# Optimization experiments

Hardware: AMD Instinct MI355X
Metric: run time of the kernel (lower is better)

Reference implementation:

```python
import jax, jax.numpy as jnp
import numpy as np

B, N, M, D = 8, 2048, 2048, 512

def setup_inputs() -> dict:
    key = jax.random.key(0)
    ks = jax.random.split(key, 10)
    s = 1.0 / np.sqrt(D)  # torch Linear default init scale (approx)
    return {
        "lidar_features": jax.random.normal(ks[0], (B, N, D), jnp.float32),
        "camera_features": jax.random.normal(ks[1], (B, M, D), jnp.float32),
        "lidar_confidence": jax.random.uniform(ks[2], (B, N, 1), jnp.float32),
        "camera_confidence": jax.random.uniform(ks[3], (B, M, 1), jnp.float32),
        "Wq": jax.random.normal(ks[4], (D, D), jnp.float32) * s,
        "bq": jnp.zeros((D,), jnp.float32),
        "Wk": jax.random.normal(ks[5], (D, D), jnp.float32) * s,
        "bk": jnp.zeros((D,), jnp.float32),
        "Wv": jax.random.normal(ks[6], (D, D), jnp.float32) * s,
        "bv": jnp.zeros((D,), jnp.float32),
    }

def reference(lidar_features, camera_features, lidar_confidence, camera_confidence,
              Wq, bq, Wk, bk, Wv, bv):
    # torch nn.Linear: x @ W.T + b
    q = (jnp.einsum('bnd,ed->bne', lidar_features, Wq) + bq) * lidar_confidence
    k = jnp.einsum('bmd,ed->bme', camera_features, Wk) + bk
    v = jnp.einsum('bmd,ed->bme', camera_features, Wv) + bv
    # note: no 1/sqrt(d) scaling in the original; camera_confidence is unused
    scores = jnp.einsum('bne,bme->bnm', q, k)  # [B,N,M]
    attn = jax.nn.softmax(scores, axis=-1)
    fused = jnp.einsum('bnm,bme->bne', attn, v)
    return fused
```

## Files before the change

kernel.cpp:

```cpp
#include <hip/hip_runtime.h>
#include <hip/hip_bf16.h>

#define BB 8
#define NN 2048
#define MM 2048
#define DD 512

typedef __attribute__((ext_vector_type(8))) _Float16 f16x8;
typedef __attribute__((ext_vector_type(4))) float f32x4;
typedef __attribute__((ext_vector_type(8))) unsigned short u16x8;

__device__ __forceinline__ unsigned short f2h(float x){
  union { _Float16 h; unsigned short u; } cv;
  cv.h = (_Float16)x;
  return cv.u;
}
__device__ __forceinline__ float h2f(unsigned short u){
  union { unsigned short u; _Float16 h; } cv;
  cv.u = u;
  return (float)cv.h;
}
__device__ __forceinline__ f32x4 mfmah(f16x8 a, f16x8 b, f32x4 c){
  return __builtin_amdgcn_mfma_f32_16x16x32_f16(a, b, c, 0, 0, 0);
}

#define GLD16(gp, lp) __builtin_amdgcn_global_load_lds( \
    (const __attribute__((address_space(1))) void*)(gp), \
    (__attribute__((address_space(3))) void*)(lp), 16, 0, 0)

#define WAITVM(n) __builtin_amdgcn_s_waitcnt(0xF70 | (n))

__device__ __forceinline__ void swz_xyz(int& bn, int& bm, int& bz){
  int f = ((int)blockIdx.z * (int)gridDim.y + (int)blockIdx.y) * (int)gridDim.x
        + (int)blockIdx.x;
  bz = f & 7;
  int r = f >> 3;
  bn = r % (int)gridDim.x;
  bm = r / (int)gridDim.x;
}

__global__ __launch_bounds__(256) void cvt16_kernel(const float* __restrict__ in,
    unsigned short* __restrict__ out, int n4){
  int i = blockIdx.x*256 + threadIdx.x;
  const int stride = gridDim.x*256;
  for (; i < n4; i += stride){
    float4 v = ((const float4*)in)[i];
    ushort4 h; h.x=f2h(v.x); h.y=f2h(v.y); h.z=f2h(v.z); h.w=f2h(v.w);
    ((ushort4*)out)[i] = h;
  }
}

__global__ __launch_bounds__(256) void cam_prep(const float* __restrict__ cam,
    const float* __restrict__ c2,
    unsigned short* __restrict__ camH,
    float* __restrict__ svec){
  const int t = threadIdx.x;
  const int l = t & 63;
  const size_t row = (size_t)blockIdx.x*4 + (t >> 6);
  const float4* r4 = (const float4*)(cam + row*DD);
  const float4* c4 = (const float4*)c2;
  float4 v0 = r4[l*2],   v1 = r4[l*2+1];
  float4 a0 = c4[l*2],   a1 = c4[l*2+1];
  float p = v0.x*a0.x + v0.y*a0.y + v0.z*a0.z + v0.w*a0.w
          + v1.x*a1.x + v1.y*a1.y + v1.z*a1.z + v1.w*a1.w;
  for (int o = 32; o; o >>= 1) p += __shfl_xor(p, o);
  if (l == 0) svec[row] = p;
  ushort4 h0; h0.x=f2h(v0.x); h0.y=f2h(v0.y); h0.z=f2h(v0.z); h0.w=f2h(v0.w);
  ushort4 h1; h1.x=f2h(v1.x); h1.y=f2h(v1.y); h1.z=f2h(v1.z); h1.w=f2h(v1.w);
  ushort4* dst = (ushort4*)(camH + row*DD);
  dst[l*2]   = h0;
  dst[l*2+1] = h1;
}

__global__ __launch_bounds__(256) void at_kernel(const float* __restrict__ Wq,
                                                 const float* __restrict__ Wk,
                                                 unsigned short* __restrict__ atH){
  const int i0 = blockIdx.x * 32, j0 = blockIdx.y * 32;
  __shared__ float q_s[32][33];
  __shared__ float k_s[32][33];
  const int t = threadIdx.x;
  const int tx = t & 15, ty = t >> 4;
  float acc[2][2] = {{0.f,0.f},{0.f,0.f}};
  for (int e0 = 0; e0 < DD; e0 += 32){
    __syncthreads();
#pragma unroll
    for (int p = 0; p < 4; ++p){
      int idx = t + 256*p;
      int e = idx >> 5, c = idx & 31;
      q_s[e][c] = Wq[(size_t)(e0+e)*DD + i0 + c];
      k_s[e][c] = Wk[(size_t)(e0+e)*DD + j0 + c];
    }
    __syncthreads();
#pragma unroll 8
    for (int e = 0; e < 32; ++e){
      float q0 = q_s[e][2*tx], q1 = q_s[e][2*tx+1];
      float k0 = k_s[e][2*ty], k1 = k_s[e][2*ty+1];
      acc[0][0] += k0*q0; acc[0][1] += k0*q1;
      acc[1][0] += k1*q0; acc[1][1] += k1*q1;
    }
  }
#pragma unroll
  for (int a = 0; a < 2; ++a)
#pragma unroll
    for (int b = 0; b < 2; ++b)
      atH[(size_t)(j0 + 2*ty + a)*DD + i0 + 2*tx + b] = f2h(acc[a][b]);
}

__global__ __launch_bounds__(256) void c2_kernel(const float* __restrict__ bq,
                                                 const float* __restrict__ Wk,
                                                 float* __restrict__ c2){
  int d = blockIdx.x * 256 + threadIdx.x;
  float a = 0.f;
  for (int e = 0; e < DD; ++e) a += bq[e] * Wk[(size_t)e*DD + d];
  c2[d] = a;
}

template<int MODE>
__global__ __launch_bounds__(256) void gemm_h128(
    const unsigned short* __restrict__ Ag, long sA, int lda,
    const unsigned short* __restrict__ Bg, long sB, int ldb,
    unsigned short* __restrict__ O, long sO, int ldo,
    const float* __restrict__ bias)
{
  __shared__ __attribute__((aligned(16))) unsigned short Ah[128][40];
  __shared__ __attribute__((aligned(16))) unsigned short Bh[128][40];

  int bn, bm, bz; swz_xyz(bn, bm, bz);
  const int t = threadIdx.x;
  const int lane = t & 63, w = t >> 6;
  const int wrow = w >> 1, wcol = w & 1;
  const int lr = lane & 15, lk = (lane >> 4) << 3;

  f32x4 acc[4][4];
#pragma unroll
  for (int m = 0; m < 4; ++m)
#pragma unroll
    for (int n = 0; n < 4; ++n){ f32x4 z = {0.f,0.f,0.f,0.f}; acc[m][n] = z; }

  const unsigned short* Ap = Ag + (size_t)bz*(size_t)sA + ((size_t)bm*128)*(size_t)lda;
  const unsigned short* Bp = Bg + (size_t)bz*(size_t)sB + ((size_t)bn*128)*(size_t)ldb;

  const int sr = t >> 2;
  const int sc = (t & 3) * 8;

  for (int k0 = 0; k0 < DD; k0 += 32){
    __syncthreads();
#pragma unroll
    for (int p = 0; p < 2; ++p){
      int r = sr + 64*p;
      *(u16x8*)&Ah[r][sc] = *(const u16x8*)(Ap + (size_t)r*lda + k0 + sc);
      *(u16x8*)&Bh[r][sc] = *(const u16x8*)(Bp + (size_t)r*ldb + k0 + sc);
    }
    __syncthreads();

    f16x8 af[4], bf[4];
#pragma unroll
    for (int m = 0; m < 4; ++m) af[m] = *(const f16x8*)&Ah[wrow*64 + m*16 + lr][lk];
#pragma unroll
    for (int n = 0; n < 4; ++n) bf[n] = *(const f16x8*)&Bh[wcol*64 + n*16 + lr][lk];
#pragma unroll
    for (int m = 0; m < 4; ++m)
#pragma unroll
      for (int n = 0; n < 4; ++n)
        acc[m][n] = mfmah(af[m], bf[n], acc[m][n]);
  }

  const int orow = bm*128 + wrow*64;
  const int ocol = bn*128 + wcol*64;
#pragma unroll
  for (int m = 0; m < 4; ++m){
#pragma unroll
    for (int n = 0; n < 4; ++n){
      int col  = ocol + n*16 + lr;
      int row0 = orow + m*16 + ((lane >> 4) << 2);
#pragma unroll
      for (int r = 0; r < 4; ++r){
        int row = row0 + r;
        float v = acc[m][n][r];
        if constexpr (MODE == 1) v += bias[row];
        O[(size_t)bz*(size_t)sO + (size_t)row*ldo + col] = f2h(v);
      }
    }
  }
}

__global__ __launch_bounds__(512) void gemm_scores(
    const unsigned short* __restrict__ Th, const unsigned short* __restrict__ camH,
    unsigned short* __restrict__ O,
    const float* __restrict__ conf, const float* __restrict__ svec)
{
  __shared__ unsigned short Ah[3][128][32];
  __shared__ unsigned short Bh[3][256][32];

  int bn, bm, bz; swz_xyz(bn, bm, bz);
  const int t = threadIdx.x;
  const int lane = t & 63, w = t >> 6;
  const int wrow = w >> 2, wcol = w & 3;
  const int lr = lane & 15;
  const int c4 = lane >> 4;

  const unsigned short* Ap = Th   + (size_t)bz*((size_t)NN*DD) + ((size_t)bm*128)*DD;
  const unsigned short* Bp = camH + (size_t)bz*((size_t)MM*DD) + ((size_t)bn*256)*DD;

  const int sar  = w*16 + (lane >> 2);
  const int salc = (lane & 3) ^ (sar & 3);
  const unsigned short* gA = Ap + (size_t)sar*DD + salc*8;
  const int sbr  = w*32 + (lane >> 2);
  const int sblc = (lane & 3) ^ (sbr & 3);
  const unsigned short* gB = Bp + (size_t)sbr*DD + sblc*8;

#define SC_STAGE(bufi, kofs) do {                                  \
    GLD16(gA + (kofs),                 &Ah[bufi][w*16     ][0]);   \
    GLD16(gB + (kofs),                 &Bh[bufi][w*32     ][0]);   \
    GLD16(gB + (kofs) + (size_t)16*DD, &Bh[bufi][w*32 + 16][0]);   \
  } while(0)

#define SC_COMPUTE(bufi) do {                                      \
    f16x8 af[4], bf[4];                                            \
    _Pragma("unroll")                                              \
    for (int m = 0; m < 4; ++m){                                   \
      int row = wrow*64 + m*16 + lr;                               \
      int pc  = c4 ^ (row & 3);                                    \
      af[m] = *(const f16x8*)&Ah[bufi][row][pc*8];                 \
    }                                                              \
    _Pragma("unroll")                                              \
    for (int n = 0; n < 4; ++n){                                   \
      int row = wcol*64 + n*16 + lr;                               \
      int pc  = c4 ^ (row & 3);                                    \
      bf[n] = *(const f16x8*)&Bh[bufi][row][pc*8];                 \
    }                                                              \
    __builtin_amdgcn_s_setprio(1);                                 \
    _Pragma("unroll")                                              \
    for (int m = 0; m < 4; ++m)                                    \
      _Pragma("unroll")                                            \
      for (int n = 0; n < 4; ++n)                                  \
        acc[m][n] = mfmah(af[m], bf[n], acc[m][n]);                \
    __builtin_amdgcn_s_setprio(0);                                 \
  } while(0)

  f32x4 acc[4][4];
#pragma unroll
  for (int m = 0; m < 4; ++m)
#pragma unroll
    for (int n = 0; n < 4; ++n){ f32x4 z = {0.f,0.f,0.f,0.f}; acc[m][n] = z; }

  SC_STAGE(0, 0);
  SC_STAGE(1, 32);

  for (int tt = 0; tt < 15; ++tt){
    WAITVM(3);
    __builtin_amdgcn_s_barrier();
    __builtin_amdgcn_sched_barrier(0);
    if (tt < 14) SC_STAGE((tt+2)%3, (size_t)(tt+2)*32);
    SC_COMPUTE(tt%3);
  }
  WAITVM(0);
  __builtin_amdgcn_s_barrier();
  __builtin_amdgcn_sched_barrier(0);
  SC_COMPUTE(0);
#undef SC_STAGE
#undef SC_COMPUTE

  const int orow0 = bm*128 + wrow*64;
  const int ocol0 = bn*256 + wcol*64;
  const size_t obase = (size_t)bz*((size_t)NN*MM);
#pragma unroll
  for (int m = 0; m < 4; ++m){
#pragma unroll
    for (int n = 0; n < 4; ++n){
      int col  = ocol0 + n*16 + lr;
      float sv = svec[bz*MM + col];
      int row0 = orow0 + m*16 + ((lane >> 4) << 2);
#pragma unroll
      for (int r = 0; r < 4; ++r){
        int row = row0 + r;
        O[obase + (size_t)row*MM + col]
            = f2h(conf[bz*NN + row] * (acc[m][n][r] + sv));
      }
    }
  }
}

__global__ __launch_bounds__(256) void softmax_h(unsigned short* __restrict__ scores){
  const size_t row = blockIdx.x;
  unsigned short* pr = scores + row * (size_t)MM;
  const int t = threadIdx.x;

  u16x8 v = ((const u16x8*)pr)[t];
  float x[8];
#pragma unroll
  for (int j = 0; j < 8; ++j) x[j] = h2f(v[j]);

  float mx = x[0];
#pragma unroll
  for (int j = 1; j < 8; ++j) mx = fmaxf(mx, x[j]);
  for (int o = 32; o; o >>= 1) mx = fmaxf(mx, __shfl_xor(mx, o));
  __shared__ float red[4];
  if ((t & 63) == 0) red[t >> 6] = mx;
  __syncthreads();
  mx = fmaxf(fmaxf(red[0], red[1]), fmaxf(red[2], red[3]));

  float e[8], s = 0.f;
#pragma unroll
  for (int j = 0; j < 8; ++j){ e[j] = __expf(x[j] - mx); s += e[j]; }
  for (int o = 32; o; o >>= 1) s += __shfl_xor(s, o);
  __syncthreads();
  if ((t & 63) == 0) red[t >> 6] = s;
  __syncthreads();
  float inv = 1.f / (red[0] + red[1] + red[2] + red[3]);

  u16x8 pv;
#pragma unroll
  for (int j = 0; j < 8; ++j) pv[j] = f2h(e[j] * inv);
  ((u16x8*)pr)[t] = pv;
}

__global__ __launch_bounds__(512) void gemm_pv(
    const unsigned short* __restrict__ P,
    const unsigned short* __restrict__ V,
    float* __restrict__ O)
{
  __shared__ unsigned short Ah[2][64][64];
  __shared__ unsigned short Bh[2][256][64];

  int bn, bm, bz; swz_xyz(bn, bm, bz);
  const int t = threadIdx.x;
  const int lane = t & 63, w = t >> 6;
  const int lr = lane & 15, lc0 = lane >> 4;

  const unsigned short* Ap = P + (size_t)bz*((size_t)NN*MM) + ((size_t)bm*64)*MM;
  const unsigned short* Bp = V + (size_t)bz*((size_t)DD*MM) + ((size_t)bn*256)*MM;

  const int arow = 8*w + (lane >> 3);
  const int alc  = (lane & 7) ^ (arow & 7);
  const unsigned short* gA = Ap + (size_t)arow*MM + alc*8;
  const int brow = 32*w + (lane >> 3);
  const int blc  = (lane & 7) ^ (brow & 7);
  const unsigned short* gB = Bp + (size_t)brow*MM + blc*8;

#define PV_STAGE(bufi, kofs) do {                                   \
    GLD16(gA + (kofs),                 &Ah[bufi][8*w][0]);          \
    GLD16(gB + (kofs),                 &Bh[bufi][32*w     ][0]);    \
    GLD16(gB + (kofs) + (size_t)8*MM,  &Bh[bufi][32*w +  8][0]);    \
    GLD16(gB + (kofs) + (size_t)16*MM, &Bh[bufi][32*w + 16][0]);    \
    GLD16(gB + (kofs) + (size_t)24*MM, &Bh[bufi][32*w + 24][0]);    \
  } while(0)

  f32x4 acc[4][2];
#pragma unroll
  for (int m = 0; m < 4; ++m)
#pragma unroll
    for (int n = 0; n < 2; ++n){ f32x4 z = {0.f,0.f,0.f,0.f}; acc[m][n] = z; }

  PV_STAGE(0, 0);
  WAITVM(0);
  __builtin_amdgcn_s_barrier();
  __builtin_amdgcn_sched_barrier(0);

  for (int tt = 0; tt < 32; ++tt){
    const int buf = tt & 1;
    if (tt < 31) PV_STAGE(buf^1, (size_t)(tt+1)*64);
    f16x8 af[4][2], bf[2][2];
#pragma unroll
    for (int m = 0; m < 4; ++m){
      int row = m*16 + lr;
#pragma unroll
      for (int ks = 0; ks < 2; ++ks){
        int pc = (ks*4 + lc0) ^ (row & 7);
        af[m][ks] = *(const f16x8*)&Ah[buf][row][pc*8];
      }
    }
#pragma unroll
    for (int n = 0; n < 2; ++n){
      int row = w*32 + n*16 + lr;
#pragma unroll
      for (int ks = 0; ks < 2; ++ks){
        int pc = (ks*4 + lc0) ^ (row & 7);
        bf[n][ks] = *(const f16x8*)&Bh[buf][row][pc*8];
      }
    }
    __builtin_amdgcn_s_setprio(1);
#pragma unroll
    for (int m = 0; m < 4; ++m)
#pragma unroll
      for (int n = 0; n < 2; ++n){
        acc[m][n] = mfmah(af[m][0], bf[n][0], acc[m][n]);
        acc[m][n] = mfmah(af[m][1], bf[n][1], acc[m][n]);
      }
    __builtin_amdgcn_s_setprio(0);

    WAITVM(0);
    __builtin_amdgcn_s_barrier();
    __builtin_amdgcn_sched_barrier(0);
  }
#undef PV_STAGE

  const int orow0 = bm*64;
  const int ocol0 = bn*256 + w*32;
#pragma unroll
  for (int m = 0; m < 4; ++m){
#pragma unroll
    for (int n = 0; n < 2; ++n){
      int col  = ocol0 + n*16 + lr;
      int row0 = orow0 + m*16 + ((lane >> 4) << 2);
#pragma unroll
      for (int r = 0; r < 4; ++r){
        int row = row0 + r;
        O[(size_t)bz*((size_t)NN*DD) + (size_t)row*DD + col] = acc[m][n][r];
      }
    }
  }
}

extern "C" void kernel_launch(void* const* d_in, const int* in_sizes, int n_in,
                              void* d_out, int out_size, void* d_ws, size_t ws_size,
                              hipStream_t stream) {
  const float* lidar  = (const float*)d_in[0];
  const float* camera = (const float*)d_in[1];
  const float* lconf  = (const float*)d_in[2];
  const float* Wq = (const float*)d_in[4];
  const float* bq = (const float*)d_in[5];
  const float* Wk = (const float*)d_in[6];
  const float* Wv = (const float*)d_in[8];
  const float* bv = (const float*)d_in[9];
  float* out = (float*)d_out;

  char* ws = (char*)d_ws;
  unsigned short* scores = (unsigned short*)(ws + 0);
  unsigned short* liH    = (unsigned short*)(ws + 0);
  unsigned short* atH    = (unsigned short*)(ws + 16777216);
  unsigned short* wvH    = (unsigned short*)(ws + 17301504);
  float*          c2     = (float*)(ws + 17825792);
  unsigned short* Th     = (unsigned short*)(ws + 134217728);
  unsigned short* camH   = (unsigned short*)(ws + 150994944);
  unsigned short* Vt     = (unsigned short*)(ws + 167772160);
  float*          svec   = (float*)(ws + 184549376);

  c2_kernel<<<dim3(2), 256, 0, stream>>>(bq, Wk, c2);
  cam_prep<<<dim3(BB*MM/4), 256, 0, stream>>>(camera, c2, camH, svec);
  cvt16_kernel<<<dim3(2048), 256, 0, stream>>>(lidar,  liH,  BB*NN*DD/4);
  cvt16_kernel<<<dim3(256),  256, 0, stream>>>(Wv,     wvH,  DD*DD/4);
  at_kernel<<<dim3(16,16), 256, 0, stream>>>(Wq, Wk, atH);

  gemm_h128<0><<<dim3(DD/128, NN/128, BB), 256, 0, stream>>>(
      liH, (long)NN*DD, DD,  atH, 0, DD,
      Th, (long)NN*DD, DD, nullptr);

  gemm_h128<1><<<dim3(MM/128, DD/128, BB), 256, 0, stream>>>(
      wvH, 0, DD,  camH, (long)MM*DD, DD,
      Vt, (long)DD*MM, MM, bv);

  gemm_scores<<<dim3(MM/256, NN/128, BB), 512, 0, stream>>>(
      Th, camH, scores, lconf, svec);

  softmax_h<<<dim3(BB*NN), 256, 0, stream>>>(scores);

  gemm_pv<<<dim3(DD/256, NN/64, BB), 512, 0, stream>>>(
      scores, Vt, out);
}
```

Before: 196.4 us.

## Enlarge PV GEMM tile to 128x256 with 4-stage shared-memory pipeline

The P·V GEMM block tile grows from 64x256 to 128x256, and the warps are rearranged as a 2x4 grid where each warp owns a 64x64 output subtile. This raises operand reuse from LDS and halves the number of re-reads of V per output row. The single double buffer with K-step 64 becomes a 4-stage ring with K-step 32 and partial vmcnt waits, so global loads run several steps ahead of compute. In exchange it uses more accumulator registers, and launches half as many blocks, which may reduce occupancy.

```diff
diff --git a/kernel.cpp b/kernel.cpp
--- a/kernel.cpp
+++ b/kernel.cpp
@@ -320,93 +320,100 @@
     const unsigned short* __restrict__ V,
     float* __restrict__ O)
 {
-  __shared__ unsigned short Ah[2][64][64];
-  __shared__ unsigned short Bh[2][256][64];
+  __shared__ unsigned short Ah[4][128][32];
+  __shared__ unsigned short Bh[4][256][32];
 
   int bn, bm, bz; swz_xyz(bn, bm, bz);
   const int t = threadIdx.x;
   const int lane = t & 63, w = t >> 6;
-  const int lr = lane & 15, lc0 = lane >> 4;
-
-  const unsigned short* Ap = P + (size_t)bz*((size_t)NN*MM) + ((size_t)bm*64)*MM;
+  const int wrow = w >> 2, wcol = w & 3;
+  const int lr = lane & 15;
+  const int c4 = lane >> 4;
+
+  const unsigned short* Ap = P + (size_t)bz*((size_t)NN*MM) + ((size_t)bm*128)*MM;
   const unsigned short* Bp = V + (size_t)bz*((size_t)DD*MM) + ((size_t)bn*256)*MM;
 
-  const int arow = 8*w + (lane >> 3);
-  const int alc  = (lane & 7) ^ (arow & 7);
-  const unsigned short* gA = Ap + (size_t)arow*MM + alc*8;
-  const int brow = 32*w + (lane >> 3);
-  const int blc  = (lane & 7) ^ (brow & 7);
-  const unsigned short* gB = Bp + (size_t)brow*MM + blc*8;
-
-#define PV_STAGE(bufi, kofs) do {                                   \
-    GLD16(gA + (kofs),                 &Ah[bufi][8*w][0]);          \
-    GLD16(gB + (kofs),                 &Bh[bufi][32*w     ][0]);    \
-    GLD16(gB + (kofs) + (size_t)8*MM,  &Bh[bufi][32*w +  8][0]);    \
-    GLD16(gB + (kofs) + (size_t)16*MM, &Bh[bufi][32*w + 16][0]);    \
-    GLD16(gB + (kofs) + (size_t)24*MM, &Bh[bufi][32*w + 24][0]);    \
+  const int sar  = w*16 + (lane >> 2);
+  const int salc = (lane & 3) ^ (sar & 3);
+  const unsigned short* gA = Ap + (size_t)sar*MM + salc*8;
+  const int sbr  = w*32 + (lane >> 2);
+  const int sblc = (lane & 3) ^ (sbr & 3);
+  const unsigned short* gB = Bp + (size_t)sbr*MM + sblc*8;
+
+#define PV_STAGE(bufi, kofs) do {                                  \
+    GLD16(gA + (kofs),                 &Ah[bufi][w*16     ][0]);   \
+    GLD16(gB + (kofs),                 &Bh[bufi][w*32     ][0]);   \
+    GLD16(gB + (kofs) + (size_t)16*MM, &Bh[bufi][w*32 + 16][0]);   \
   } while(0)
 
-  f32x4 acc[4][2];
+#define PV_COMPUTE(bufi) do {                                      \
+    f16x8 af[4], bf[4];                                            \
+    _Pragma("unroll")                                              \
+    for (int m = 0; m < 4; ++m){                                   \
+      int row = wrow*64 + m*16 + lr;                               \
+      int pc  = c4 ^ (row & 3);                                    \
+      af[m] = *(const f16x8*)&Ah[bufi][row][pc*8];                 \
+    }                                                              \
+    _Pragma("unroll")                                              \
+    for (int n = 0; n < 4; ++n){                                   \
+      int row = wcol*64 + n*16 + lr;                               \
+      int pc  = c4 ^ (row & 3);                                    \
+      bf[n] = *(const f16x8*)&Bh[bufi][row][pc*8];                 \
+    }                                                              \
+    __builtin_amdgcn_s_setprio(1);                                 \
+    _Pragma("unroll")                                              \
+    for (int m = 0; m < 4; ++m)                                    \
+      _Pragma("unroll")                                            \
+      for (int n = 0; n < 4; ++n)                                  \
+        acc[m][n] = mfmah(af[m], bf[n], acc[m][n]);                \
+    __builtin_amdgcn_s_setprio(0);                                 \
+  } while(0)
+
+  f32x4 acc[4][4];
 #pragma unroll
   for (int m = 0; m < 4; ++m)
 #pragma unroll
-    for (int n = 0; n < 2; ++n){ f32x4 z = {0.f,0.f,0.f,0.f}; acc[m][n] = z; }
+    for (int n = 0; n < 4; ++n){ f32x4 z = {0.f,0.f,0.f,0.f}; acc[m][n] = z; }
 
   PV_STAGE(0, 0);
+  PV_STAGE(1, 32);
+  PV_STAGE(2, 64);
+
+  for (int tt = 0; tt < 61; ++tt){
+    WAITVM(6);
+    __builtin_amdgcn_s_barrier();
+    __builtin_amdgcn_sched_barrier(0);
+    PV_STAGE((tt+3)&3, (size_t)(tt+3)*32);
+    PV_COMPUTE(tt&3);
+  }
+  WAITVM(6);
+  __builtin_amdgcn_s_barrier();
+  __builtin_amdgcn_sched_barrier(0);
+  PV_COMPUTE(1);
+  WAITVM(3);
+  __builtin_amdgcn_s_barrier();
+  __builtin_amdgcn_sched_barrier(0);
+  PV_COMPUTE(2);
   WAITVM(0);
   __builtin_amdgcn_s_barrier();
   __builtin_amdgcn_sched_barrier(0);
-
-  for (int tt = 0; tt < 32; ++tt){
-    const int buf = tt & 1;
-    if (tt < 31) PV_STAGE(buf^1, (size_t)(tt+1)*64);
-    f16x8 af[4][2], bf[2][2];
-#pragma unroll
-    for (int m = 0; m < 4; ++m){
-      int row = m*16 + lr;
-#pragma unroll
-      for (int ks = 0; ks < 2; ++ks){
-        int pc = (ks*4 + lc0) ^ (row & 7);
-        af[m][ks] = *(const f16x8*)&Ah[buf][row][pc*8];
-      }
-    }
-#pragma unroll
-    for (int n = 0; n < 2; ++n){
-      int row = w*32 + n*16 + lr;
-#pragma unroll
-      for (int ks = 0; ks < 2; ++ks){
-        int pc = (ks*4 + lc0) ^ (row & 7);
-        bf[n][ks] = *(const f16x8*)&Bh[buf][row][pc*8];
-      }
-    }
-    __builtin_amdgcn_s_setprio(1);
-#pragma unroll
-    for (int m = 0; m < 4; ++m)
-#pragma unroll
-      for (int n = 0; n < 2; ++n){
-        acc[m][n] = mfmah(af[m][0], bf[n][0], acc[m][n]);
-        acc[m][n] = mfmah(af[m][1], bf[n][1], acc[m][n]);
-      }
-    __builtin_amdgcn_s_setprio(0);
-
-    WAITVM(0);
-    __builtin_amdgcn_s_barrier();
-    __builtin_amdgcn_sched_barrier(0);
-  }
+  PV_COMPUTE(3);
 #undef PV_STAGE
-
-  const int orow0 = bm*64;
-  const int ocol0 = bn*256 + w*32;
+#undef PV_COMPUTE
+
+  const int orow0 = bm*128 + wrow*64;
+  const int ocol0 = bn*256 + wcol*64;
+  const size_t obase = (size_t)bz*((size_t)NN*DD);
 #pragma unroll
   for (int m = 0; m < 4; ++m){
 #pragma unroll
-    for (int n = 0; n < 2; ++n){
+    for (int n = 0; n < 4; ++n){
       int col  = ocol0 + n*16 + lr;
       int row0 = orow0 + m*16 + ((lane >> 4) << 2);
 #pragma unroll
       for (int r = 0; r < 4; ++r){
         int row = row0 + r;
-        O[(size_t)bz*((size_t)NN*DD) + (size_t)row*DD + col] = acc[m][n][r];
+        O[obase + (size_t)row*DD + col] = acc[m][n][r];
       }
     }
   }
@@ -455,6 +462,6 @@
 
   softmax_h<<<dim3(BB*NN), 256, 0, stream>>>(scores);
 
-  gemm_pv<<<dim3(DD/256, NN/64, BB), 512, 0, stream>>>(
+  gemm_pv<<<dim3(DD/256, NN/128, BB), 512, 0, stream>>>(
       scores, Vt, out);
 }
```

Result: slower. 216.7 us (+10.3%).

## Rewrite projection GEMMs with async double-buffered swizzled LDS pipeline

Applied to the files above, without the earlier changes.

The two projection GEMMs move from a 128x128 tile with synchronous global-to-LDS copies to a 64x256 tile with 512 threads, using direct global-to-LDS loads into double-buffered XOR-swizzled shared memory, the same scheme the PV kernel already uses. The next k-tile is prefetched while MFMAs run on the current one, and wave priority is raised around the MFMA block. This targets load latency and LDS bank conflicts in the Q-side and V projections. It also changes the tile shape and grid size, which affects occupancy and how often operands are reused.

```diff
diff --git a/kernel.cpp b/kernel.cpp
--- a/kernel.cpp
+++ b/kernel.cpp
@@ -116,63 +116,95 @@
 }
 
 template<int MODE>
-__global__ __launch_bounds__(256) void gemm_h128(
+__global__ __launch_bounds__(512) void gemm_h256(
     const unsigned short* __restrict__ Ag, long sA, int lda,
     const unsigned short* __restrict__ Bg, long sB, int ldb,
     unsigned short* __restrict__ O, long sO, int ldo,
     const float* __restrict__ bias)
 {
-  __shared__ __attribute__((aligned(16))) unsigned short Ah[128][40];
-  __shared__ __attribute__((aligned(16))) unsigned short Bh[128][40];
+  __shared__ unsigned short Ah[2][64][64];
+  __shared__ unsigned short Bh[2][256][64];
 
   int bn, bm, bz; swz_xyz(bn, bm, bz);
   const int t = threadIdx.x;
   const int lane = t & 63, w = t >> 6;
-  const int wrow = w >> 1, wcol = w & 1;
-  const int lr = lane & 15, lk = (lane >> 4) << 3;
-
-  f32x4 acc[4][4];
+  const int lr = lane & 15, lc0 = lane >> 4;
+
+  const unsigned short* Ap = Ag + (size_t)bz*(size_t)sA + ((size_t)bm*64)*(size_t)lda;
+  const unsigned short* Bp = Bg + (size_t)bz*(size_t)sB + ((size_t)bn*256)*(size_t)ldb;
+
+  const int arow = 8*w + (lane >> 3);
+  const int alc  = (lane & 7) ^ (arow & 7);
+  const unsigned short* gA = Ap + (size_t)arow*lda + alc*8;
+  const int brow = 32*w + (lane >> 3);
+  const int blc  = (lane & 7) ^ (brow & 7);
+  const unsigned short* gB = Bp + (size_t)brow*ldb + blc*8;
+
+#define H_STAGE(bufi, kofs) do {                                     \
+    GLD16(gA + (kofs),                  &Ah[bufi][8*w][0]);          \
+    GLD16(gB + (kofs),                  &Bh[bufi][32*w     ][0]);    \
+    GLD16(gB + (kofs) + (size_t)8*ldb,  &Bh[bufi][32*w +  8][0]);    \
+    GLD16(gB + (kofs) + (size_t)16*ldb, &Bh[bufi][32*w + 16][0]);    \
+    GLD16(gB + (kofs) + (size_t)24*ldb, &Bh[bufi][32*w + 24][0]);    \
+  } while(0)
+
+  f32x4 acc[4][2];
 #pragma unroll
   for (int m = 0; m < 4; ++m)
 #pragma unroll
-    for (int n = 0; n < 4; ++n){ f32x4 z = {0.f,0.f,0.f,0.f}; acc[m][n] = z; }
-
-  const unsigned short* Ap = Ag + (size_t)bz*(size_t)sA + ((size_t)bm*128)*(size_t)lda;
-  const unsigned short* Bp = Bg + (size_t)bz*(size_t)sB + ((size_t)bn*128)*(size_t)ldb;
-
-  const int sr = t >> 2;
-  const int sc = (t & 3) * 8;
-
-  for (int k0 = 0; k0 < DD; k0 += 32){
-    __syncthreads();
-#pragma unroll
-    for (int p = 0; p < 2; ++p){
-      int r = sr + 64*p;
-      *(u16x8*)&Ah[r][sc] = *(const u16x8*)(Ap + (size_t)r*lda + k0 + sc);
-      *(u16x8*)&Bh[r][sc] = *(const u16x8*)(Bp + (size_t)r*ldb + k0 + sc);
-    }
-    __syncthreads();
-
-    f16x8 af[4], bf[4];
-#pragma unroll
-    for (int m = 0; m < 4; ++m) af[m] = *(const f16x8*)&Ah[wrow*64 + m*16 + lr][lk];
-#pragma unroll
-    for (int n = 0; n < 4; ++n) bf[n] = *(const f16x8*)&Bh[wcol*64 + n*16 + lr][lk];
+    for (int n = 0; n < 2; ++n){ f32x4 z = {0.f,0.f,0.f,0.f}; acc[m][n] = z; }
+
+  H_STAGE(0, 0);
+  WAITVM(0);
+  __builtin_amdgcn_s_barrier();
+  __builtin_amdgcn_sched_barrier(0);
+
+  for (int tt = 0; tt < 8; ++tt){
+    const int buf = tt & 1;
+    if (tt < 7) H_STAGE(buf^1, (size_t)(tt+1)*64);
+    f16x8 af[4][2], bf[2][2];
+#pragma unroll
+    for (int m = 0; m < 4; ++m){
+      int row = m*16 + lr;
+#pragma unroll
+      for (int ks = 0; ks < 2; ++ks){
+        int pc = (ks*4 + lc0) ^ (row & 7);
+        af[m][ks] = *(const f16x8*)&Ah[buf][row][pc*8];
+      }
+    }
+#pragma unroll
+    for (int n = 0; n < 2; ++n){
+      int row = w*32 + n*16 + lr;
+#pragma unroll
+      for (int ks = 0; ks < 2; ++ks){
+        int pc = (ks*4 + lc0) ^ (row & 7);
+        bf[n][ks] = *(const f16x8*)&Bh[buf][row][pc*8];
+      }
+    }
+    __builtin_amdgcn_s_setprio(1);
 #pragma unroll
     for (int m = 0; m < 4; ++m)
 #pragma unroll
-      for (int n = 0; n < 4; ++n)
-        acc[m][n] = mfmah(af[m], bf[n], acc[m][n]);
-  }
-
-  const int orow = bm*128 + wrow*64;
-  const int ocol = bn*128 + wcol*64;
+      for (int n = 0; n < 2; ++n){
+        acc[m][n] = mfmah(af[m][0], bf[n][0], acc[m][n]);
+        acc[m][n] = mfmah(af[m][1], bf[n][1], acc[m][n]);
+      }
+    __builtin_amdgcn_s_setprio(0);
+
+    WAITVM(0);
+    __builtin_amdgcn_s_barrier();
+    __builtin_amdgcn_sched_barrier(0);
+  }
+#undef H_STAGE
+
+  const int orow0 = bm*64;
+  const int ocol0 = bn*256 + w*32;
 #pragma unroll
   for (int m = 0; m < 4; ++m){
 #pragma unroll
-    for (int n = 0; n < 4; ++n){
-      int col  = ocol + n*16 + lr;
-      int row0 = orow + m*16 + ((lane >> 4) << 2);
+    for (int n = 0; n < 2; ++n){
+      int col  = ocol0 + n*16 + lr;
+      int row0 = orow0 + m*16 + ((lane >> 4) << 2);
 #pragma unroll
       for (int r = 0; r < 4; ++r){
         int row = row0 + r;
@@ -360,6 +392,7 @@
   for (int tt = 0; tt < 32; ++tt){
     const int buf = tt & 1;
     if (tt < 31) PV_STAGE(buf^1, (size_t)(tt+1)*64);
+
     f16x8 af[4][2], bf[2][2];
 #pragma unroll
     for (int m = 0; m < 4; ++m){
@@ -442,11 +475,11 @@
   cvt16_kernel<<<dim3(256),  256, 0, stream>>>(Wv,     wvH,  DD*DD/4);
   at_kernel<<<dim3(16,16), 256, 0, stream>>>(Wq, Wk, atH);
 
-  gemm_h128<0><<<dim3(DD/128, NN/128, BB), 256, 0, stream>>>(
+  gemm_h256<0><<<dim3(DD/256, NN/64, BB), 512, 0, stream>>>(
       liH, (long)NN*DD, DD,  atH, 0, DD,
       Th, (long)NN*DD, DD, nullptr);
 
-  gemm_h128<1><<<dim3(MM/128, DD/128, BB), 256, 0, stream>>>(
+  gemm_h256<1><<<dim3(MM/256, DD/64, BB), 512, 0, stream>>>(
       wvH, 0, DD,  camH, (long)MM*DD, DD,
       Vt, (long)DD*MM, MM, bv);
 
```

New measurement: 197.3 us. No clear change (+0.5%).
